# Kernel tuning notes

Hardware: AMD Instinct MI355X
Metric: run time of the kernel (lower is better)

The kernel has to match this reference:

```python
import jax, jax.numpy as jnp
import numpy as np

N = 102400          # input_size (mesh nodes)
SFC = 2             # number of space-filling curves
K, S, P = 32, 4, 16 # kernel_size, stride, padding (= K//2)
OPADS = [1, 1, 1, 0]  # decoder output paddings per convT layer
NFC = 16            # num_final_channels
L0 = 401            # inv_conv_start
SIZE_FC = [12832, 1024, 128]
B = 64
# convT layer j: ConvTranspose1d(channels[-j] -> channels[-j-1]); channels=[1,8,16,16,16]
CONV_IO = [(16, 16), (16, 16), (16, 8), (8, 1)]


def conv_transpose1d(x, w, b, stride, padding, output_padding):
    # x: (B, Cin, L); w: torch layout (Cin, Cout, K)
    k = w.shape[-1]
    w_conv = jnp.flip(w, -1).transpose(1, 0, 2)  # (Cout, Cin, K)
    out = jax.lax.conv_general_dilated(
        x, w_conv, window_strides=(1,),
        padding=[(k - 1 - padding, k - 1 - padding + output_padding)],
        lhs_dilation=(stride,),
        dimension_numbers=('NCH', 'OIH', 'NCH'))
    return out + b[None, :, None]


def setup_inputs() -> dict:
    key = jax.random.key(0)
    ks = jax.random.split(key, 12)
    f32 = jnp.float32

    def nrm(k, shape, scale):
        return jax.random.normal(k, shape, f32) * scale

    # inverse SFC orderings: permutations of [0, N); plus/minus neighbours per repo helpers
    rng = np.random.RandomState(0)
    inv = np.stack([rng.permutation(N) for _ in range(SFC)]).astype(np.int32)
    plus = np.concatenate([inv[:, 1:], inv[:, -1:]], axis=1)   # find_plus_neigh
    minus = np.concatenate([inv[:, :1], inv[:, :-1]], axis=1)  # find_minus_neigh

    inp = {
        'x': nrm(ks[0], (B, SIZE_FC[2]), 1.0),
        'fc_w1': nrm(ks[1], (SIZE_FC[1], SIZE_FC[2]), 0.05),
        'fc_b1': jnp.full((SIZE_FC[1],), 0.001, f32),
        'fc_w2': nrm(ks[2], (SIZE_FC[0], SIZE_FC[1]), 0.02),
        'fc_b2': jnp.full((SIZE_FC[0],), 0.001, f32),
        'nn_w': jnp.full((SFC, N, 3), 1.0 / 3.0, f32) + nrm(ks[3], (SFC, N, 3), 0.01),
        'nn_b': jnp.zeros((SFC, N), f32),
        'ord_idx': jnp.asarray(inv),
        'minus_idx': jnp.asarray(minus),
        'plus_idx': jnp.asarray(plus),
    }
    for j, (cin, cout) in enumerate(CONV_IO):
        inp[f'conv_w{j+1}'] = nrm(ks[4 + j], (SFC, cin, cout, K), 0.03)
        inp[f'conv_b{j+1}'] = jnp.full((SFC, cout), 0.001, f32)
    return inp


def reference(x, fc_w1, fc_b1, fc_w2, fc_b2,
              conv_w1, conv_b1, conv_w2, conv_b2,
              conv_w3, conv_b3, conv_w4, conv_b4,
              nn_w, nn_b, ord_idx, minus_idx, plus_idx):
    act = jnp.tanh
    conv_ws = [conv_w1, conv_w2, conv_w3, conv_w4]
    conv_bs = [conv_b1, conv_b2, conv_b3, conv_b4]

    # FC stack (decoder walks size_fc in reverse)
    h = act(x @ fc_w1.T + fc_b1)
    h = act(h @ fc_w2.T + fc_b2)
    h = h.reshape(-1, SIZE_FC[0] // SFC, SFC)  # (B, split, sfc_nums)

    z = None
    for i in range(SFC):
        b = h[..., i].reshape(-1, NFC, L0)  # (B, 16, 401)
        for j in range(len(conv_ws)):
            b = act(conv_transpose1d(b, conv_ws[j][i], conv_bs[j][i], S, P, OPADS[j]))
        b = b.reshape(-1, N)  # (B, N)
        # SFC gather of (minus, self, plus) neighbours + NearestNeighbouring weighted sum
        tt = jnp.stack([b[:, minus_idx[i]], b[:, ord_idx[i]], b[:, plus_idx[i]]], axis=-1)  # (B, N, 3)
        z_i = act(jnp.einsum('bnm,nm->bn', tt, nn_w[i]) + nn_b[i])
        z = z_i if z is None else z + z_i
    return act(z)  # sfc_nums > 1: sum over curves then activate
```

## Files before the change

kernel.cpp:

```cpp
#include <hip/hip_runtime.h>

#define NNODES 102400

__device__ __forceinline__ float ftanh(float x) {
    float a = fabsf(x);
    float e = __expf(-2.0f * a);
    float t = (1.0f - e) / (1.0f + e);
    return copysignf(t, x);
}

__global__ __launch_bounds__(256) void fc1_kernel(
    const float* __restrict__ x, const float* __restrict__ w1,
    const float* __restrict__ b1, float* __restrict__ h1t)
{
    const int b = threadIdx.x & 63;
    const int o = blockIdx.x * 4 + __builtin_amdgcn_readfirstlane(threadIdx.x >> 6);
    const float* xr = x + b * 128;
    const float* wr = w1 + o * 128;
    float acc = 0.f;
#pragma unroll
    for (int k = 0; k < 128; ++k) acc = fmaf(xr[k], wr[k], acc);
    h1t[o * 64 + b] = ftanh(acc + b1[o]);
}

__global__ __launch_bounds__(128) void fc2_gemm_kernel(
    const float* __restrict__ h1t,
    const float* __restrict__ w2,
    float* __restrict__ part)
{
    __shared__ float Wl[32][68];
    __shared__ float Hl[64][64];
    const int t  = threadIdx.x;
    const int o0 = blockIdx.x * 32;
    const int ks = blockIdx.y;
    const int ob = (t >> 4) * 4;
    const int b4 = (t & 15) * 4;

    float acc[4][4] = {};
    const int kbase = ks * 256;
#pragma unroll 1
    for (int kt = 0; kt < 4; ++kt) {
        const int k0 = kbase + kt * 64;
        {
            const int row = t >> 2;
            const int c0  = (t & 3) * 4;
            const float* src = w2 + (size_t)(o0 + row) * 1024 + k0;
#pragma unroll
            for (int i = 0; i < 4; ++i) {
                const float4 v = *reinterpret_cast<const float4*>(src + c0 + 16 * i);
                *reinterpret_cast<float4*>(&Wl[row][c0 + 16 * i]) = v;
            }
        }
        {
            const float* src = h1t + (size_t)k0 * 64;
            float* dst = &Hl[0][0];
#pragma unroll
            for (int i = 0; i < 8; ++i) {
                const int f4 = t + 128 * i;
                const float4 v = *reinterpret_cast<const float4*>(src + f4 * 4);
                *reinterpret_cast<float4*>(dst + f4 * 4) = v;
            }
        }
        __syncthreads();
#pragma unroll
        for (int kk = 0; kk < 16; ++kk) {
            const int k4 = kk * 4;
            float wv[4][4], hv[4][4];
#pragma unroll
            for (int i = 0; i < 4; ++i) {
                const float4 v = *reinterpret_cast<const float4*>(&Wl[ob + i][k4]);
                wv[i][0] = v.x; wv[i][1] = v.y; wv[i][2] = v.z; wv[i][3] = v.w;
            }
#pragma unroll
            for (int j = 0; j < 4; ++j) {
                const float4 v = *reinterpret_cast<const float4*>(&Hl[k4 + j][b4]);
                hv[j][0] = v.x; hv[j][1] = v.y; hv[j][2] = v.z; hv[j][3] = v.w;
            }
#pragma unroll
            for (int i = 0; i < 4; ++i)
#pragma unroll
                for (int j = 0; j < 4; ++j)
#pragma unroll
                    for (int jb = 0; jb < 4; ++jb)
                        acc[i][jb] = fmaf(wv[i][j], hv[j][jb], acc[i][jb]);
        }
        __syncthreads();
    }
    float* pb = part + ((size_t)ks * 12832 + o0) * 64;
#pragma unroll
    for (int i = 0; i < 4; ++i) {
        const float4 v = make_float4(acc[i][0], acc[i][1], acc[i][2], acc[i][3]);
        *reinterpret_cast<float4*>(pb + (size_t)(ob + i) * 64 + b4) = v;
    }
}

__global__ __launch_bounds__(256) void fc2_reduce_kernel(
    const float* __restrict__ part, const float* __restrict__ b2,
    float* __restrict__ h2t)
{
    const int idx = blockIdx.x * 256 + threadIdx.x;
    const int o = idx >> 6;
    const float s = part[idx] + part[821248 + idx]
                  + part[1642496 + idx] + part[2463744 + idx];
    h2t[idx] = ftanh(s + b2[o]);
}

__device__ __forceinline__ void pack_one(const float* __restrict__ w, float* __restrict__ wp,
                                         int CIN, int COUT, int idx)
{
    const int k = idx & 31;
    int r = idx >> 5;
    const int co = r % COUT; r /= COUT;
    const int ci = r % CIN;
    const int i  = r / CIN;
    const int k0 = k & 3, d = k >> 2;
    wp[(((i * 4 + k0) * 8 + d) * CIN + ci) * COUT + co] = w[idx];
}

__global__ __launch_bounds__(256) void pack_all_kernel(
    const float* __restrict__ w1, const float* __restrict__ w2,
    const float* __restrict__ w3, const float* __restrict__ w4,
    float* __restrict__ wp1, float* __restrict__ wp2,
    float* __restrict__ wp3, float* __restrict__ wp4)
{
    const int idx = blockIdx.x * 256 + threadIdx.x;
    if (idx < 16384)       pack_one(w1, wp1, 16, 16, idx);
    else if (idx < 32768)  pack_one(w2, wp2, 16, 16, idx - 16384);
    else if (idx < 40960)  pack_one(w3, wp3, 16,  8, idx - 32768);
    else if (idx < 41472)  pack_one(w4, wp4,  8,  1, idx - 40960);
}

template<int CIN, int CPG, int TT, int JSTR, bool GUARD>
__device__ __forceinline__ void conv_core(
    const float* __restrict__ xs, int cistride, int Lin,
    const float* __restrict__ wk, int wco, int jhi0, float (&acc)[TT][CPG])
{
    constexpr int NJ = TT + 7;
    const int jlo = jhi0 - 7;
    const float* xsj = xs + (ptrdiff_t)jlo * JSTR;
    for (int ci = 0; ci < CIN; ++ci) {
        float xv[NJ];
        if constexpr (GUARD) {
            const float* xpc = xs + (size_t)ci * cistride;
#pragma unroll
            for (int q = 0; q < NJ; ++q) {
                const int j = jlo + q;
                xv[q] = (j >= 0 && j < Lin) ? xpc[(ptrdiff_t)j * JSTR] : 0.f;
            }
        } else {
            const float* xpc = xsj + (size_t)ci * cistride;
#pragma unroll
            for (int q = 0; q < NJ; ++q)
                xv[q] = xpc[q * JSTR];
        }
        const float* wc = wk + ci * wco;
#pragma unroll
        for (int d = 0; d < 8; ++d) {
            const float* wd = wc + d * CIN * wco;
            float wv[CPG];
            if constexpr ((CPG & 3) == 0) {
#pragma unroll
                for (int cq = 0; cq < CPG; cq += 4) {
                    const float4 w4 = *reinterpret_cast<const float4*>(wd + cq);
                    wv[cq + 0] = w4.x; wv[cq + 1] = w4.y;
                    wv[cq + 2] = w4.z; wv[cq + 3] = w4.w;
                }
            } else {
#pragma unroll
                for (int co = 0; co < CPG; ++co) wv[co] = wd[co];
            }
#pragma unroll
            for (int tt = 0; tt < TT; ++tt) {
                const float xx = xv[7 + tt - d];
#pragma unroll
                for (int co = 0; co < CPG; ++co)
                    acc[tt][co] = fmaf(xx, wv[co], acc[tt][co]);
            }
        }
    }
}

template<int CIN, int COUT, int TT, int COG, int MINW, int JSTR>
__global__ __launch_bounds__(256, MINW) void convt3_kernel(
    const float* __restrict__ x, size_t sfc_xstride, int cistride,
    const float* __restrict__ wp, int sfc_wstride,
    const float* __restrict__ bias, int sfc_bstride,
    float* __restrict__ y, size_t sfc_ystride,
    int Lin, int Lout)
{
    constexpr int CPG = COUT / COG;
    const int b = threadIdx.x & 63;
    const int widx = __builtin_amdgcn_readfirstlane(threadIdx.x >> 6);
    const int t0 = blockIdx.x * (4 * TT) + widx;
    if (t0 >= Lout) return;
    const int cb = blockIdx.z * CPG;
    const int k0   = (t0 + 16) & 3;
    const int jhi0 = (t0 + 16) >> 2;
    const float* xs = x + (size_t)blockIdx.y * sfc_xstride + b;
    const float* wk = wp + blockIdx.y * sfc_wstride + k0 * (8 * CIN * COUT) + cb;
    const float* bs = bias + blockIdx.y * sfc_bstride + cb;

    float acc[TT][CPG];
#pragma unroll
    for (int co = 0; co < CPG; ++co) {
        const float bv = bs[co];
#pragma unroll
        for (int tt = 0; tt < TT; ++tt) acc[tt][co] = bv;
    }

    const bool interior = (jhi0 >= 7) && (jhi0 + TT - 1 < Lin);
    if (interior)
        conv_core<CIN, CPG, TT, JSTR, false>(xs, cistride, Lin, wk, COUT, jhi0, acc);
    else
        conv_core<CIN, CPG, TT, JSTR, true >(xs, cistride, Lin, wk, COUT, jhi0, acc);

#pragma unroll
    for (int tt = 0; tt < TT; ++tt) {
        const int t = t0 + 4 * tt;
        if (t < Lout) {
#pragma unroll
            for (int co = 0; co < CPG; ++co)
                y[(size_t)blockIdx.y * sfc_ystride + ((size_t)(cb + co) * Lout + t) * 64 + b] =
                    ftanh(acc[tt][co]);
        }
    }
}

template<int CIN, int TT, bool GUARD>
__device__ __forceinline__ void conv4_core(
    const float* __restrict__ xs, int cistride, int Lin, int jhi0,
    const float (&wreg)[8][CIN], float (&acc)[TT])
{
    constexpr int NJ = TT + 7;
    const int jlo = jhi0 - 7;
    const float* xsj = xs + (ptrdiff_t)jlo * 64;
    for (int ci = 0; ci < CIN; ++ci) {
        float xv[NJ];
        if constexpr (GUARD) {
            const float* xpc = xs + (size_t)ci * cistride;
#pragma unroll
            for (int q = 0; q < NJ; ++q) {
                const int j = jlo + q;
                xv[q] = (j >= 0 && j < Lin) ? xpc[(ptrdiff_t)j * 64] : 0.f;
            }
        } else {
            const float* xpc = xsj + (size_t)ci * cistride;
#pragma unroll
            for (int q = 0; q < NJ; ++q)
                xv[q] = xpc[q * 64];
        }
#pragma unroll
        for (int d = 0; d < 8; ++d)
#pragma unroll
            for (int tt = 0; tt < TT; ++tt)
                acc[tt] = fmaf(xv[7 + tt - d], wreg[d][ci], acc[tt]);
    }
}

template<int CIN, int TT, int MINW>
__global__ __launch_bounds__(256, MINW) void convt4_kernel(
    const float* __restrict__ x, size_t sfc_xstride, int cistride,
    const float* __restrict__ wp, int sfc_wstride,
    const float* __restrict__ bias, int sfc_bstride,
    float* __restrict__ y, size_t sfc_ystride, int Lin, int Lout)
{
    const int b = threadIdx.x & 63;
    const int widx = __builtin_amdgcn_readfirstlane(threadIdx.x >> 6);
    const int t0 = blockIdx.x * (4 * TT) + widx;
    if (t0 >= Lout) return;
    const int k0   = (t0 + 16) & 3;
    const int jhi0 = (t0 + 16) >> 2;
    const float* wk = wp + blockIdx.y * sfc_wstride + k0 * (8 * CIN);
    float wreg[8][CIN];
#pragma unroll
    for (int d = 0; d < 8; ++d)
#pragma unroll
        for (int ci = 0; ci < CIN; ++ci)
            wreg[d][ci] = wk[d * CIN + ci];
    const float bv = bias[blockIdx.y * sfc_bstride];
    float acc[TT];
#pragma unroll
    for (int tt = 0; tt < TT; ++tt) acc[tt] = bv;
    const float* xs = x + (size_t)blockIdx.y * sfc_xstride + b;

    const bool interior = (jhi0 >= 7) && (jhi0 + TT - 1 < Lin);
    if (interior) conv4_core<CIN, TT, false>(xs, cistride, Lin, jhi0, wreg, acc);
    else          conv4_core<CIN, TT, true >(xs, cistride, Lin, jhi0, wreg, acc);

    float* yb = y + (size_t)blockIdx.y * sfc_ystride;
#pragma unroll
    for (int tt = 0; tt < TT; ++tt) {
        const int t = t0 + 4 * tt;
        if (t < Lout) yb[(size_t)t * 64 + b] = ftanh(acc[tt]);
    }
}

__global__ __launch_bounds__(256) void final_kernel(
    const float* __restrict__ d0, const float* __restrict__ d1,
    const float* __restrict__ nn_w, const float* __restrict__ nn_b,
    const int* __restrict__ oi,
    float* __restrict__ out)
{
    __shared__ float zl[16][65];
    const int tid = threadIdx.x;
    const int b = tid & 63;
    const int widx = __builtin_amdgcn_readfirstlane(tid >> 6);
    const int nblk = blockIdx.x * 16;
    const int n0 = nblk + widx * 4;

    float g[2][6];
#pragma unroll
    for (int s = 0; s < 2; ++s) {
        const float* dd = s ? d1 : d0;
        const int* ois = oi + s * NNODES;
#pragma unroll
        for (int q = 0; q < 6; ++q) {
            int pos = n0 - 1 + q;
            pos = pos < 0 ? 0 : (pos > NNODES - 1 ? NNODES - 1 : pos);
            g[s][q] = dd[(size_t)ois[pos] * 64 + b];
        }
    }
#pragma unroll
    for (int nn = 0; nn < 4; ++nn) {
        const int n = n0 + nn;
        float z = 0.f;
#pragma unroll
        for (int s = 0; s < 2; ++s) {
            const float* wv = nn_w + (size_t)(s * NNODES + n) * 3;
            z += ftanh(wv[0] * g[s][nn] + wv[1] * g[s][nn + 1]
                     + wv[2] * g[s][nn + 2] + nn_b[s * NNODES + n]);
        }
        zl[widx * 4 + nn][b] = ftanh(z);
    }
    __syncthreads();
    const int bq = tid >> 2;
    const int nq = tid & 3;
    float4 v;
    v.x = zl[nq * 4 + 0][bq];
    v.y = zl[nq * 4 + 1][bq];
    v.z = zl[nq * 4 + 2][bq];
    v.w = zl[nq * 4 + 3][bq];
    *reinterpret_cast<float4*>(out + (size_t)bq * NNODES + nblk + nq * 4) = v;
}

extern "C" void kernel_launch(void* const* d_in, const int* in_sizes, int n_in,
                              void* d_out, int out_size, void* d_ws, size_t ws_size,
                              hipStream_t stream)
{
    const float* x     = (const float*)d_in[0];
    const float* fc_w1 = (const float*)d_in[1];
    const float* fc_b1 = (const float*)d_in[2];
    const float* fc_w2 = (const float*)d_in[3];
    const float* fc_b2 = (const float*)d_in[4];
    const float* nn_w  = (const float*)d_in[5];
    const float* nn_b  = (const float*)d_in[6];
    const int* ord_i   = (const int*)d_in[7];
    const int* minus_i = (const int*)d_in[8];
    const int* plus_i  = (const int*)d_in[9];
    const float* conv_w1 = (const float*)d_in[10];
    const float* conv_b1 = (const float*)d_in[11];
    const float* conv_w2 = (const float*)d_in[12];
    const float* conv_b2 = (const float*)d_in[13];
    const float* conv_w3 = (const float*)d_in[14];
    const float* conv_b3 = (const float*)d_in[15];
    const float* conv_w4 = (const float*)d_in[16];
    const float* conv_b4 = (const float*)d_in[17];
    float* out = (float*)d_out;
    (void)minus_i; (void)plus_i;

    const size_t SZ_Y1 = (size_t)16 * 1601 * 64;
    const size_t SZ_Y2 = (size_t)16 * 6401 * 64;
    const size_t SZ_Y3 = (size_t)8  * 25601 * 64;
    const size_t SZ_Y4 = (size_t)NNODES * 64;

    const size_t need22 = 56638976ull * 4;
    const size_t need21 = 43531264ull * 4;
    int NS = 1, NY3 = 1;
    if (ws_size >= need22)      { NS = 2; NY3 = 2; }
    else if (ws_size >= need21) { NS = 2; NY3 = 1; }

    float* ws  = (float*)d_ws;
    float* h1t = ws;
    float* h2t = h1t + 65536;
    float* y1  = h2t + 821248;
    float* y2  = y1  + (size_t)NS * SZ_Y1;
    float* y3  = y2  + (size_t)NS * SZ_Y2;
    float* y4  = y3  + (size_t)NY3 * SZ_Y3;
    float* wp1 = y4  + 2 * SZ_Y4;
    float* wp2 = wp1 + 16384;
    float* wp3 = wp2 + 16384;
    float* wp4 = wp3 + 8192;
    float* part = y3;

    fc1_kernel<<<dim3(256),  dim3(256), 0, stream>>>(x, fc_w1, fc_b1, h1t);
    fc2_gemm_kernel<<<dim3(401, 4), dim3(128), 0, stream>>>(h1t, fc_w2, part);
    fc2_reduce_kernel<<<dim3(3208), dim3(256), 0, stream>>>(part, fc_b2, h2t);
    pack_all_kernel<<<dim3(162), dim3(256), 0, stream>>>(
        conv_w1, conv_w2, conv_w3, conv_w4, wp1, wp2, wp3, wp4);

    for (int s0 = 0; s0 < 2; s0 += NS) {
        convt3_kernel<16, 16, 1, 2, 8, 128><<<dim3(401, NS, 2), dim3(256), 0, stream>>>(
            h2t + s0 * 64, 64, 401 * 128,
            wp1 + s0 * 8192, 8192, conv_b1 + s0 * 16, 16,
            y1, SZ_Y1, 401, 1601);
        convt3_kernel<16, 16, 4, 2, 6, 64><<<dim3(401, NS, 2), dim3(256), 0, stream>>>(
            y1, SZ_Y1, 1601 * 64,
            wp2 + s0 * 8192, 8192, conv_b2 + s0 * 16, 16,
            y2, SZ_Y2, 1601, 6401);
        if (NY3 == 1) {
            for (int s = s0; s < s0 + NS; ++s) {
                const float* xin = y2 + (size_t)(NS == 2 ? (s - s0) : 0) * SZ_Y2;
                convt3_kernel<16, 8, 4, 1, 8, 64><<<dim3(1601, 1, 1), dim3(256), 0, stream>>>(
                    xin, 0, 6401 * 64,
                    wp3 + s * 4096, 0, conv_b3 + s * 8, 0,
                    y3, 0, 6401, 25601);
                convt4_kernel<8, 16, 8><<<dim3(1600, 1), dim3(256), 0, stream>>>(
                    y3, 0, 25601 * 64,
                    wp4 + s * 256, 0, conv_b4 + s, 0,
                    y4 + (size_t)s * SZ_Y4, 0, 25601, 102400);
            }
        }
    }
    if (NY3 == 2) {
        convt3_kernel<16, 8, 4, 1, 8, 64><<<dim3(1601, 2, 1), dim3(256), 0, stream>>>(
            y2, SZ_Y2, 6401 * 64,
            wp3, 4096, conv_b3, 8,
            y3, SZ_Y3, 6401, 25601);
        convt4_kernel<8, 16, 8><<<dim3(1600, 2), dim3(256), 0, stream>>>(
            y3, SZ_Y3, 25601 * 64,
            wp4, 256, conv_b4, 1,
            y4, SZ_Y4, 25601, 102400);
    }

    final_kernel<<<dim3(6400), dim3(256), 0, stream>>>(
        y4, y4 + SZ_Y4, nn_w, nn_b, ord_i, out);
}
```

Before: 289.0 us.

## Stage layer-3 transposed-conv input tile in LDS with 512-thread blocks

Adds a dedicated kernel for the third transposed convolution (16 to 8 channels) that cooperatively loads a 15-row input window for all 16 input channels into shared memory with float4 loads. Each of the 8 waves then computes 4 output positions by 8 channels from LDS. This replaces per-thread global reads, which overlap between neighbouring outputs, with a single staged load per block, aiming to cut redundant global and L2 traffic. The cost is about 61 KB of LDS per block and a barrier, which may limit occupancy. Unused minus/plus index variables are also removed.

```diff
diff --git a/kernel.cpp b/kernel.cpp
--- a/kernel.cpp
+++ b/kernel.cpp
@@ -226,6 +226,91 @@
     }
 }
 
+__global__ __launch_bounds__(512, 4) void convt3_lds_kernel(
+    const float* __restrict__ x, size_t sfc_xstride,
+    const float* __restrict__ wp, int sfc_wstride,
+    const float* __restrict__ bias, int sfc_bstride,
+    float* __restrict__ y, size_t sfc_ystride,
+    int Lin, int Lout)
+{
+    constexpr int CIN = 16, CO = 8, TT = 4, NROW = 15;
+    __shared__ float Xl[CIN][NROW][64];
+    const int tid = threadIdx.x;
+    const int T0 = blockIdx.x * 32;
+    const int J0 = (T0 + 16) >> 2;
+    const int jbase = J0 - 7;
+    const float* xb = x + (size_t)blockIdx.y * sfc_xstride;
+
+#pragma unroll
+    for (int it = 0; it < 8; ++it) {
+        const int f = tid + it * 512;
+        if (f < CIN * NROW * 16) {
+            const int c4  = f & 15;
+            const int row = (f >> 4) % NROW;
+            const int ci  = (f >> 4) / NROW;
+            const int j = jbase + row;
+            float4 v = make_float4(0.f, 0.f, 0.f, 0.f);
+            if (j >= 0 && j < Lin)
+                v = *reinterpret_cast<const float4*>(xb + ((size_t)ci * Lin + j) * 64 + c4 * 4);
+            *reinterpret_cast<float4*>(&Xl[ci][row][c4 * 4]) = v;
+        }
+    }
+    __syncthreads();
+
+    const int b = tid & 63;
+    const int w = __builtin_amdgcn_readfirstlane(tid >> 6);
+    const int k0 = w & 3;
+    const int h  = w >> 2;
+    const int t0 = T0 + 16 * h + k0;
+    const float* wk = wp + blockIdx.y * sfc_wstride + k0 * (8 * CIN * CO);
+    const float* bs = bias + blockIdx.y * sfc_bstride;
+
+    float acc[TT][CO];
+#pragma unroll
+    for (int co = 0; co < CO; ++co) {
+        const float bv = bs[co];
+#pragma unroll
+        for (int tt = 0; tt < TT; ++tt) acc[tt][co] = bv;
+    }
+
+    for (int ci = 0; ci < CIN; ++ci) {
+        float xv[11];
+#pragma unroll
+        for (int q = 0; q < 11; ++q)
+            xv[q] = Xl[ci][4 * h + q][b];
+        const float* wc = wk + ci * CO;
+#pragma unroll
+        for (int d = 0; d < 8; ++d) {
+            const float* wd = wc + d * CIN * CO;
+            float wv[CO];
+#pragma unroll
+            for (int cq = 0; cq < CO; cq += 4) {
+                const float4 w4 = *reinterpret_cast<const float4*>(wd + cq);
+                wv[cq + 0] = w4.x; wv[cq + 1] = w4.y;
+                wv[cq + 2] = w4.z; wv[cq + 3] = w4.w;
+            }
+#pragma unroll
+            for (int tt = 0; tt < TT; ++tt) {
+                const float xx = xv[7 + tt - d];
+#pragma unroll
+                for (int co = 0; co < CO; ++co)
+                    acc[tt][co] = fmaf(xx, wv[co], acc[tt][co]);
+            }
+        }
+    }
+
+    float* yb = y + (size_t)blockIdx.y * sfc_ystride;
+#pragma unroll
+    for (int tt = 0; tt < TT; ++tt) {
+        const int t = t0 + 4 * tt;
+        if (t < Lout) {
+#pragma unroll
+            for (int co = 0; co < CO; ++co)
+                yb[((size_t)co * Lout + t) * 64 + b] = ftanh(acc[tt][co]);
+        }
+    }
+}
+
 template<int CIN, int TT, bool GUARD>
 __device__ __forceinline__ void conv4_core(
     const float* __restrict__ xs, int cistride, int Lin, int jhi0,
@@ -355,8 +440,6 @@
     const float* nn_w  = (const float*)d_in[5];
     const float* nn_b  = (const float*)d_in[6];
     const int* ord_i   = (const int*)d_in[7];
-    const int* minus_i = (const int*)d_in[8];
-    const int* plus_i  = (const int*)d_in[9];
     const float* conv_w1 = (const float*)d_in[10];
     const float* conv_b1 = (const float*)d_in[11];
     const float* conv_w2 = (const float*)d_in[12];
@@ -366,7 +449,6 @@
     const float* conv_w4 = (const float*)d_in[16];
     const float* conv_b4 = (const float*)d_in[17];
     float* out = (float*)d_out;
-    (void)minus_i; (void)plus_i;
 
     const size_t SZ_Y1 = (size_t)16 * 1601 * 64;
     const size_t SZ_Y2 = (size_t)16 * 6401 * 64;
@@ -410,8 +492,8 @@
         if (NY3 == 1) {
             for (int s = s0; s < s0 + NS; ++s) {
                 const float* xin = y2 + (size_t)(NS == 2 ? (s - s0) : 0) * SZ_Y2;
-                convt3_kernel<16, 8, 4, 1, 8, 64><<<dim3(1601, 1, 1), dim3(256), 0, stream>>>(
-                    xin, 0, 6401 * 64,
+                convt3_lds_kernel<<<dim3(801, 1), dim3(512), 0, stream>>>(
+                    xin, 0,
                     wp3 + s * 4096, 0, conv_b3 + s * 8, 0,
                     y3, 0, 6401, 25601);
                 convt4_kernel<8, 16, 8><<<dim3(1600, 1), dim3(256), 0, stream>>>(
@@ -422,8 +504,8 @@
         }
     }
     if (NY3 == 2) {
-        convt3_kernel<16, 8, 4, 1, 8, 64><<<dim3(1601, 2, 1), dim3(256), 0, stream>>>(
-            y2, SZ_Y2, 6401 * 64,
+        convt3_lds_kernel<<<dim3(801, 2), dim3(512), 0, stream>>>(
+            y2, SZ_Y2,
             wp3, 4096, conv_b3, 8,
             y3, SZ_Y3, 6401, 25601);
         convt4_kernel<8, 16, 8><<<dim3(1600, 2), dim3(256), 0, stream>>>(
```

New measurement: 318.4 us. +10.2%, slower.
